# Kernel optimization log

Measured on AMD Instinct MI355X. Metric: run time of the kernel, lower is better.

## Reference

```python
import jax, jax.numpy as jnp
import numpy as np

DEPTH = 4096
BATCH = 16384


def fwht(x):
    """Normalized fast Walsh-Hadamard transform along the last axis.
    x: [B, n], n a power of two. Returns H @ x rows, scaled by 1/sqrt(n).
    """
    B, n = x.shape
    h = 1
    while h < n:
        # combine elements i and i+h within blocks of size 2h (butterfly)
        x = x.reshape(B, n // (2 * h), 2, h)
        a = x[..., 0, :]
        b = x[..., 1, :]
        x = jnp.concatenate([a + b, a - b], axis=-1).reshape(B, n)
        h *= 2
    return x * (1.0 / jnp.sqrt(jnp.asarray(n, x.dtype)))


def setup_inputs() -> dict:
    key = jax.random.key(0)
    kx, kp = jax.random.split(key)
    x = jax.random.normal(kx, (BATCH, DEPTH), dtype=jnp.float32)
    # learned diagonal vectors S, G, B initialized to ones as in the module
    diag_s = jnp.ones((DEPTH,), dtype=jnp.float32)
    diag_g = jnp.ones((DEPTH,), dtype=jnp.float32)
    diag_b = jnp.ones((DEPTH,), dtype=jnp.float32)
    # random permutation: torch.mm(y, P) with P a row-permuted identity is a
    # column gather y[:, idx] for idx = argsort(pi); idx itself is a uniform
    # random permutation, so we draw it directly.
    perm_idx = jax.random.permutation(kp, jnp.arange(DEPTH, dtype=jnp.int32))
    return {"x": x, "diag_s": diag_s, "diag_g": diag_g, "diag_b": diag_b,
            "perm_idx": perm_idx}


def reference(x, diag_s, diag_g, diag_b, perm_idx):
    # forward: S * H * G * P * H * B  (dropout in eval mode -> identity)
    y = x * diag_b                 # mul_b: diagonal scale
    y = fwht(y)                    # first Walsh-Hadamard transform
    y = jnp.take(y, perm_idx, axis=1)  # mul_p: column permutation
    y = y * diag_g                 # mul_g
    y = fwht(y)                    # second Walsh-Hadamard transform
    y = y * diag_s                 # mul_s
    return y
```

## Files before the change

### kernel.cpp

```cpp
#include <hip/hip_runtime.h>

#define FF_N 4096
#define S64  0.015625f

typedef float v2f __attribute__((ext_vector_type(2)));

__device__ __forceinline__ v2f pk_add(v2f a, v2f b) {
    v2f d; asm("v_pk_add_f32 %0, %1, %2" : "=v"(d) : "v"(a), "v"(b)); return d;
}
__device__ __forceinline__ v2f pk_sub(v2f a, v2f b) {
    v2f d; asm("v_pk_add_f32 %0, %1, %2 neg_lo:[0,1] neg_hi:[0,1]"
               : "=v"(d) : "v"(a), "v"(b)); return d;
}

__device__ __forceinline__ void h16p(v2f v[16]) {
#pragma unroll
    for (int b = 1; b < 16; b <<= 1) {
#pragma unroll
        for (int r = 0; r < 16; ++r) {
            if ((r & b) == 0) {
                const v2f u = v[r], w = v[r | b];
                v[r]     = pk_add(u, w);
                v[r | b] = pk_sub(u, w);
            }
        }
    }
}

__global__ void ff_setup(const float* __restrict__ diag_s,
                         const float* __restrict__ diag_g,
                         const int*   __restrict__ perm,
                         int*   __restrict__ gaddr2,
                         float* __restrict__ gg,
                         float* __restrict__ ss) {
    const int k   = blockIdx.x * 256 + threadIdx.x;
    const int pe  = perm[k];
    const int d2p = pe >> 8, d1p = (pe >> 4) & 15, d0p = pe & 15;
    gaddr2[k] = 512 * (d2p >> 1) + 32 * d1p + 2 * (d0p ^ ((d2p >> 1) & 7)) + (d2p & 1);
    gg[k] = diag_g[k] * S64;
    ss[k] = diag_s[k] * S64;
}

__global__ __launch_bounds__(256) void fastfood_pk_kernel(
    const float* __restrict__ x,
    const float* __restrict__ diag_b,
    const int*   __restrict__ gaddr2,
    const float* __restrict__ gg,
    const float* __restrict__ ss,
    float* __restrict__ out)
{
    __shared__ __align__(16) v2f lds2[FF_N];
    const int t = threadIdx.x;
    const int T = t >> 4, c = t & 15;
    const int h = c >> 3;
    const size_t rowA = (size_t)blockIdx.x * 2;
    const float* __restrict__ xA   = x   + rowA * FF_N;
    const float* __restrict__ xB   = xA  + FF_N;
    float* __restrict__       outA = out + rowA * FF_N;
    float* __restrict__       outB = outA + FF_N;

    v2f v2[16];

    {
        const float4* __restrict__ xa4 = (const float4*)(xA + 16 * t);
        const float4* __restrict__ xb4 = (const float4*)(xB + 16 * t);
        const float4* __restrict__ b4  = (const float4*)(diag_b + 16 * t);
#pragma unroll
        for (int q = 0; q < 4; ++q) {
            const float4 bv = b4[q];
            const float4 av = xa4[q];
            const float4 wv = xb4[q];
            v2[4 * q + 0][0] = av.x * bv.x;  v2[4 * q + 0][1] = wv.x * bv.x;
            v2[4 * q + 1][0] = av.y * bv.y;  v2[4 * q + 1][1] = wv.y * bv.y;
            v2[4 * q + 2][0] = av.z * bv.z;  v2[4 * q + 2][1] = wv.z * bv.z;
            v2[4 * q + 3][0] = av.w * bv.w;  v2[4 * q + 3][1] = wv.w * bv.w;
        }
        h16p(v2);
#pragma unroll
        for (int m = 0; m < 8; ++m) {
            const int p = 256 * c + 16 * T + 2 * (m ^ (c & 7));
            *(float4*)&lds2[p] = make_float4(v2[2 * m][0], v2[2 * m][1],
                                             v2[2 * m + 1][0], v2[2 * m + 1][1]);
        }
    }
    __syncthreads();

#pragma unroll
    for (int j = 0; j < 16; ++j)
        v2[j] = lds2[256 * j + 16 * T + 2 * ((c >> 1) ^ (j & 7)) + (c & 1)];
    h16p(v2);
    __syncthreads();
#pragma unroll
    for (int m = 0; m < 8; ++m) {
        const int p = 256 * T + 32 * m + 2 * c;
        const v2f lo = h ? v2[2 * m + 1] : v2[2 * m];
        const v2f hi = h ? v2[2 * m]     : v2[2 * m + 1];
        *(float4*)&lds2[p] = make_float4(lo[0], lo[1], hi[0], hi[1]);
    }
    __syncthreads();

#pragma unroll
    for (int j = 0; j < 16; ++j)
        v2[j] = lds2[256 * j + 32 * (T >> 1) + 2 * c + ((T & 1) ^ h)];
    h16p(v2);
    __syncthreads();
#pragma unroll
    for (int mu = 0; mu < 8; ++mu) {
        const int p = 512 * mu + 32 * T + 2 * (c ^ (mu & 7));
        *(float4*)&lds2[p] = make_float4(v2[2 * mu][0], v2[2 * mu][1],
                                         v2[2 * mu + 1][0], v2[2 * mu + 1][1]);
    }
    __syncthreads();

    {
        const int4*   __restrict__ ga4 = (const int4*)(gaddr2 + 16 * t);
        const float4* __restrict__ gg4 = (const float4*)(gg + 16 * t);
#pragma unroll
        for (int q = 0; q < 4; ++q) {
            const int4   pa = ga4[q];
            const float4 gv = gg4[q];
            const v2f a0 = lds2[pa.x], a1 = lds2[pa.y];
            const v2f a2 = lds2[pa.z], a3 = lds2[pa.w];
            v2[4 * q + 0][0] = a0[0] * gv.x;  v2[4 * q + 0][1] = a0[1] * gv.x;
            v2[4 * q + 1][0] = a1[0] * gv.y;  v2[4 * q + 1][1] = a1[1] * gv.y;
            v2[4 * q + 2][0] = a2[0] * gv.z;  v2[4 * q + 2][1] = a2[1] * gv.z;
            v2[4 * q + 3][0] = a3[0] * gv.w;  v2[4 * q + 3][1] = a3[1] * gv.w;
        }
        h16p(v2);
    }
    __syncthreads();
#pragma unroll
    for (int m = 0; m < 8; ++m) {
        const int p = 256 * c + 16 * T + 2 * (m ^ (c & 7));
        *(float4*)&lds2[p] = make_float4(v2[2 * m][0], v2[2 * m][1],
                                         v2[2 * m + 1][0], v2[2 * m + 1][1]);
    }
    __syncthreads();

#pragma unroll
    for (int j = 0; j < 16; ++j)
        v2[j] = lds2[256 * j + 16 * T + 2 * ((c >> 1) ^ (j & 7)) + (c & 1)];
    h16p(v2);
    __syncthreads();
#pragma unroll
    for (int m = 0; m < 8; ++m) {
        const int p = 256 * T + 32 * m + 2 * c;
        const v2f lo = h ? v2[2 * m + 1] : v2[2 * m];
        const v2f hi = h ? v2[2 * m]     : v2[2 * m + 1];
        *(float4*)&lds2[p] = make_float4(lo[0], lo[1], hi[0], hi[1]);
    }
    __syncthreads();

#pragma unroll
    for (int j = 0; j < 16; ++j)
        v2[j] = lds2[256 * j + 32 * (T >> 1) + 2 * c + ((T & 1) ^ h)];
    h16p(v2);
#pragma unroll
    for (int j = 0; j < 16; ++j) {
        const int e = 256 * j + t;
        const float s = ss[e];
        __builtin_nontemporal_store(v2[j][0] * s, &outA[e]);
        __builtin_nontemporal_store(v2[j][1] * s, &outB[e]);
    }
}

extern "C" void kernel_launch(void* const* d_in, const int* in_sizes, int n_in,
                              void* d_out, int out_size, void* d_ws, size_t ws_size,
                              hipStream_t stream) {
    const float* x      = (const float*)d_in[0];
    const float* diag_s = (const float*)d_in[1];
    const float* diag_g = (const float*)d_in[2];
    const float* diag_b = (const float*)d_in[3];
    const int*   perm   = (const int*)d_in[4];
    float* out = (float*)d_out;

    int*   gaddr2 = (int*)d_ws;
    float* gg     = (float*)d_ws + FF_N;
    float* ss     = (float*)d_ws + 2 * FF_N;

    ff_setup<<<FF_N / 256, 256, 0, stream>>>(diag_s, diag_g, perm, gaddr2, gg, ss);

    const int batch = in_sizes[0] / FF_N;
    fastfood_pk_kernel<<<batch / 2, 256, 0, stream>>>(x, diag_b, gaddr2, gg, ss, out);
}
```

Measured before the change: 94.26 us.

## Process four rows per block using two packed LDS buffers

Each block now handles four rows instead of two, keeping two packed register arrays and two 32 KB LDS buffers. The aim is to amortize barriers, the diag_b/gaddr/gg/ss loads and the per-block overhead over twice the work, and to give each wave more independent memory and ALU work between syncs. The cost is doubled LDS (64 KB per block) and register pressure, which lowers occupancy and halves the grid size.

```diff
diff --git a/kernel.cpp b/kernel.cpp
--- a/kernel.cpp
+++ b/kernel.cpp
@@ -24,6 +24,47 @@
                 v[r | b] = pk_sub(u, w);
             }
         }
+    }
+}
+
+__device__ __forceinline__ void a_read(v2f v[16], const v2f* __restrict__ L,
+                                       int T, int c) {
+#pragma unroll
+    for (int j = 0; j < 16; ++j)
+        v[j] = L[256 * j + 16 * T + 2 * ((c >> 1) ^ (j & 7)) + (c & 1)];
+}
+__device__ __forceinline__ void a_write(const v2f v[16], v2f* __restrict__ L,
+                                        int T, int c) {
+#pragma unroll
+    for (int m = 0; m < 8; ++m) {
+        const int p = 256 * c + 16 * T + 2 * (m ^ (c & 7));
+        *(float4*)&L[p] = make_float4(v[2 * m][0], v[2 * m][1],
+                                      v[2 * m + 1][0], v[2 * m + 1][1]);
+    }
+}
+__device__ __forceinline__ void p_read(v2f v[16], const v2f* __restrict__ L,
+                                       int T, int c, int h) {
+#pragma unroll
+    for (int j = 0; j < 16; ++j)
+        v[j] = L[256 * j + 32 * (T >> 1) + 2 * c + ((T & 1) ^ h)];
+}
+__device__ __forceinline__ void p_write(const v2f v[16], v2f* __restrict__ L,
+                                        int T, int c, int h) {
+#pragma unroll
+    for (int m = 0; m < 8; ++m) {
+        const int p = 256 * T + 32 * m + 2 * c;
+        const v2f lo = h ? v[2 * m + 1] : v[2 * m];
+        const v2f hi = h ? v[2 * m]     : v[2 * m + 1];
+        *(float4*)&L[p] = make_float4(lo[0], lo[1], hi[0], hi[1]);
+    }
+}
+__device__ __forceinline__ void w_write(const v2f v[16], v2f* __restrict__ L,
+                                        int T, int c) {
+#pragma unroll
+    for (int mu = 0; mu < 8; ++mu) {
+        const int p = 512 * mu + 32 * T + 2 * (c ^ (mu & 7));
+        *(float4*)&L[p] = make_float4(v[2 * mu][0], v[2 * mu][1],
+                                      v[2 * mu + 1][0], v[2 * mu + 1][1]);
     }
 }
 
@@ -41,7 +82,7 @@
     ss[k] = diag_s[k] * S64;
 }
 
-__global__ __launch_bounds__(256) void fastfood_pk_kernel(
+__global__ __launch_bounds__(256) void fastfood_2p_kernel(
     const float* __restrict__ x,
     const float* __restrict__ diag_b,
     const int*   __restrict__ gaddr2,
@@ -49,67 +90,62 @@
     const float* __restrict__ ss,
     float* __restrict__ out)
 {
-    __shared__ __align__(16) v2f lds2[FF_N];
+    __shared__ __align__(16) v2f LP[FF_N];
+    __shared__ __align__(16) v2f LQ[FF_N];
     const int t = threadIdx.x;
     const int T = t >> 4, c = t & 15;
     const int h = c >> 3;
-    const size_t rowA = (size_t)blockIdx.x * 2;
-    const float* __restrict__ xA   = x   + rowA * FF_N;
-    const float* __restrict__ xB   = xA  + FF_N;
-    float* __restrict__       outA = out + rowA * FF_N;
-    float* __restrict__       outB = outA + FF_N;
-
-    v2f v2[16];
+    const size_t row0 = (size_t)blockIdx.x * 4;
+    const float* __restrict__ xA = x + row0 * FF_N;
+    const float* __restrict__ xB = xA + FF_N;
+    const float* __restrict__ xC = xB + FF_N;
+    const float* __restrict__ xD = xC + FF_N;
+    float* __restrict__ oA = out + row0 * FF_N;
+    float* __restrict__ oB = oA + FF_N;
+    float* __restrict__ oC = oB + FF_N;
+    float* __restrict__ oD = oC + FF_N;
+
+    v2f vP[16], vQ[16];
 
     {
-        const float4* __restrict__ xa4 = (const float4*)(xA + 16 * t);
-        const float4* __restrict__ xb4 = (const float4*)(xB + 16 * t);
-        const float4* __restrict__ b4  = (const float4*)(diag_b + 16 * t);
+        const float4* __restrict__ a4 = (const float4*)(xA + 16 * t);
+        const float4* __restrict__ b4 = (const float4*)(xB + 16 * t);
+        const float4* __restrict__ c4 = (const float4*)(xC + 16 * t);
+        const float4* __restrict__ d4 = (const float4*)(xD + 16 * t);
+        const float4* __restrict__ g4 = (const float4*)(diag_b + 16 * t);
 #pragma unroll
         for (int q = 0; q < 4; ++q) {
-            const float4 bv = b4[q];
-            const float4 av = xa4[q];
-            const float4 wv = xb4[q];
-            v2[4 * q + 0][0] = av.x * bv.x;  v2[4 * q + 0][1] = wv.x * bv.x;
-            v2[4 * q + 1][0] = av.y * bv.y;  v2[4 * q + 1][1] = wv.y * bv.y;
-            v2[4 * q + 2][0] = av.z * bv.z;  v2[4 * q + 2][1] = wv.z * bv.z;
-            v2[4 * q + 3][0] = av.w * bv.w;  v2[4 * q + 3][1] = wv.w * bv.w;
+            const float4 gv = g4[q];
+            const float4 av = a4[q], bv = b4[q], cv = c4[q], dv = d4[q];
+            vP[4 * q + 0][0] = av.x * gv.x;  vP[4 * q + 0][1] = bv.x * gv.x;
+            vP[4 * q + 1][0] = av.y * gv.y;  vP[4 * q + 1][1] = bv.y * gv.y;
+            vP[4 * q + 2][0] = av.z * gv.z;  vP[4 * q + 2][1] = bv.z * gv.z;
+            vP[4 * q + 3][0] = av.w * gv.w;  vP[4 * q + 3][1] = bv.w * gv.w;
+            vQ[4 * q + 0][0] = cv.x * gv.x;  vQ[4 * q + 0][1] = dv.x * gv.x;
+            vQ[4 * q + 1][0] = cv.y * gv.y;  vQ[4 * q + 1][1] = dv.y * gv.y;
+            vQ[4 * q + 2][0] = cv.z * gv.z;  vQ[4 * q + 2][1] = dv.z * gv.z;
+            vQ[4 * q + 3][0] = cv.w * gv.w;  vQ[4 * q + 3][1] = dv.w * gv.w;
         }
-        h16p(v2);
-#pragma unroll
-        for (int m = 0; m < 8; ++m) {
-            const int p = 256 * c + 16 * T + 2 * (m ^ (c & 7));
-            *(float4*)&lds2[p] = make_float4(v2[2 * m][0], v2[2 * m][1],
-                                             v2[2 * m + 1][0], v2[2 * m + 1][1]);
-        }
-    }
-    __syncthreads();
-
-#pragma unroll
-    for (int j = 0; j < 16; ++j)
-        v2[j] = lds2[256 * j + 16 * T + 2 * ((c >> 1) ^ (j & 7)) + (c & 1)];
-    h16p(v2);
-    __syncthreads();
-#pragma unroll
-    for (int m = 0; m < 8; ++m) {
-        const int p = 256 * T + 32 * m + 2 * c;
-        const v2f lo = h ? v2[2 * m + 1] : v2[2 * m];
-        const v2f hi = h ? v2[2 * m]     : v2[2 * m + 1];
-        *(float4*)&lds2[p] = make_float4(lo[0], lo[1], hi[0], hi[1]);
-    }
-    __syncthreads();
-
-#pragma unroll
-    for (int j = 0; j < 16; ++j)
-        v2[j] = lds2[256 * j + 32 * (T >> 1) + 2 * c + ((T & 1) ^ h)];
-    h16p(v2);
-    __syncthreads();
-#pragma unroll
-    for (int mu = 0; mu < 8; ++mu) {
-        const int p = 512 * mu + 32 * T + 2 * (c ^ (mu & 7));
-        *(float4*)&lds2[p] = make_float4(v2[2 * mu][0], v2[2 * mu][1],
-                                         v2[2 * mu + 1][0], v2[2 * mu + 1][1]);
-    }
+        h16p(vP); h16p(vQ);
+        a_write(vP, LP, T, c);
+        a_write(vQ, LQ, T, c);
+    }
+    __syncthreads();
+
+    a_read(vP, LP, T, c);
+    a_read(vQ, LQ, T, c);
+    h16p(vP); h16p(vQ);
+    __syncthreads();
+    p_write(vP, LP, T, c, h);
+    p_write(vQ, LQ, T, c, h);
+    __syncthreads();
+
+    p_read(vP, LP, T, c, h);
+    p_read(vQ, LQ, T, c, h);
+    h16p(vP); h16p(vQ);
+    __syncthreads();
+    w_write(vP, LP, T, c);
+    w_write(vQ, LQ, T, c);
     __syncthreads();
 
     {
@@ -119,48 +155,43 @@
         for (int q = 0; q < 4; ++q) {
             const int4   pa = ga4[q];
             const float4 gv = gg4[q];
-            const v2f a0 = lds2[pa.x], a1 = lds2[pa.y];
-            const v2f a2 = lds2[pa.z], a3 = lds2[pa.w];
-            v2[4 * q + 0][0] = a0[0] * gv.x;  v2[4 * q + 0][1] = a0[1] * gv.x;
-            v2[4 * q + 1][0] = a1[0] * gv.y;  v2[4 * q + 1][1] = a1[1] * gv.y;
-            v2[4 * q + 2][0] = a2[0] * gv.z;  v2[4 * q + 2][1] = a2[1] * gv.z;
-            v2[4 * q + 3][0] = a3[0] * gv.w;  v2[4 * q + 3][1] = a3[1] * gv.w;
+            const v2f p0 = LP[pa.x], p1 = LP[pa.y], p2 = LP[pa.z], p3 = LP[pa.w];
+            const v2f q0 = LQ[pa.x], q1 = LQ[pa.y], q2 = LQ[pa.z], q3 = LQ[pa.w];
+            vP[4 * q + 0][0] = p0[0] * gv.x;  vP[4 * q + 0][1] = p0[1] * gv.x;
+            vP[4 * q + 1][0] = p1[0] * gv.y;  vP[4 * q + 1][1] = p1[1] * gv.y;
+            vP[4 * q + 2][0] = p2[0] * gv.z;  vP[4 * q + 2][1] = p2[1] * gv.z;
+            vP[4 * q + 3][0] = p3[0] * gv.w;  vP[4 * q + 3][1] = p3[1] * gv.w;
+            vQ[4 * q + 0][0] = q0[0] * gv.x;  vQ[4 * q + 0][1] = q0[1] * gv.x;
+            vQ[4 * q + 1][0] = q1[0] * gv.y;  vQ[4 * q + 1][1] = q1[1] * gv.y;
+            vQ[4 * q + 2][0] = q2[0] * gv.z;  vQ[4 * q + 2][1] = q2[1] * gv.z;
+            vQ[4 * q + 3][0] = q3[0] * gv.w;  vQ[4 * q + 3][1] = q3[1] * gv.w;
         }
-        h16p(v2);
-    }
-    __syncthreads();
-#pragma unroll
-    for (int m = 0; m < 8; ++m) {
-        const int p = 256 * c + 16 * T + 2 * (m ^ (c & 7));
-        *(float4*)&lds2[p] = make_float4(v2[2 * m][0], v2[2 * m][1],
-                                         v2[2 * m + 1][0], v2[2 * m + 1][1]);
-    }
-    __syncthreads();
-
-#pragma unroll
-    for (int j = 0; j < 16; ++j)
-        v2[j] = lds2[256 * j + 16 * T + 2 * ((c >> 1) ^ (j & 7)) + (c & 1)];
-    h16p(v2);
-    __syncthreads();
-#pragma unroll
-    for (int m = 0; m < 8; ++m) {
-        const int p = 256 * T + 32 * m + 2 * c;
-        const v2f lo = h ? v2[2 * m + 1] : v2[2 * m];
-        const v2f hi = h ? v2[2 * m]     : v2[2 * m + 1];
-        *(float4*)&lds2[p] = make_float4(lo[0], lo[1], hi[0], hi[1]);
-    }
-    __syncthreads();
-
-#pragma unroll
-    for (int j = 0; j < 16; ++j)
-        v2[j] = lds2[256 * j + 32 * (T >> 1) + 2 * c + ((T & 1) ^ h)];
-    h16p(v2);
+        h16p(vP); h16p(vQ);
+    }
+    __syncthreads();
+    a_write(vP, LP, T, c);
+    a_write(vQ, LQ, T, c);
+    __syncthreads();
+
+    a_read(vP, LP, T, c);
+    a_read(vQ, LQ, T, c);
+    h16p(vP); h16p(vQ);
+    __syncthreads();
+    p_write(vP, LP, T, c, h);
+    p_write(vQ, LQ, T, c, h);
+    __syncthreads();
+
+    p_read(vP, LP, T, c, h);
+    p_read(vQ, LQ, T, c, h);
+    h16p(vP); h16p(vQ);
 #pragma unroll
     for (int j = 0; j < 16; ++j) {
         const int e = 256 * j + t;
         const float s = ss[e];
-        __builtin_nontemporal_store(v2[j][0] * s, &outA[e]);
-        __builtin_nontemporal_store(v2[j][1] * s, &outB[e]);
+        __builtin_nontemporal_store(vP[j][0] * s, &oA[e]);
+        __builtin_nontemporal_store(vP[j][1] * s, &oB[e]);
+        __builtin_nontemporal_store(vQ[j][0] * s, &oC[e]);
+        __builtin_nontemporal_store(vQ[j][1] * s, &oD[e]);
     }
 }
 
@@ -181,5 +212,5 @@
     ff_setup<<<FF_N / 256, 256, 0, stream>>>(diag_s, diag_g, perm, gaddr2, gg, ss);
 
     const int batch = in_sizes[0] / FF_N;
-    fastfood_pk_kernel<<<batch / 2, 256, 0, stream>>>(x, diag_b, gaddr2, gg, ss, out);
-}
+    fastfood_2p_kernel<<<batch / 4, 256, 0, stream>>>(x, diag_b, gaddr2, gg, ss, out);
+}
```

Result: slower. 114.8 us (+21.8%).

## Store inter-stage FWHT data in LDS as packed fp16 pairs

Applied to the files above, without the earlier changes.

Intermediate butterfly results exchanged through shared memory are converted to packed half precision, halving LDS footprint and traffic. The LDS index layout and the permutation address table are redesigned for the 32-bit packed words, with a unified write pattern. Launch bounds now request higher occupancy. This trades accuracy (fp16 rounding at six exchange points) for lower LDS pressure, on a kernel that is largely bound by global memory bandwidth.

```diff
diff --git a/kernel.cpp b/kernel.cpp
--- a/kernel.cpp
+++ b/kernel.cpp
@@ -3,7 +3,8 @@
 #define FF_N 4096
 #define S64  0.015625f
 
-typedef float v2f __attribute__((ext_vector_type(2)));
+typedef float  v2f __attribute__((ext_vector_type(2)));
+typedef __fp16 pkhalf2 __attribute__((ext_vector_type(2)));
 
 __device__ __forceinline__ v2f pk_add(v2f a, v2f b) {
     v2f d; asm("v_pk_add_f32 %0, %1, %2" : "=v"(d) : "v"(a), "v"(b)); return d;
@@ -12,7 +13,6 @@
     v2f d; asm("v_pk_add_f32 %0, %1, %2 neg_lo:[0,1] neg_hi:[0,1]"
                : "=v"(d) : "v"(a), "v"(b)); return d;
 }
-
 __device__ __forceinline__ void h16p(v2f v[16]) {
 #pragma unroll
     for (int b = 1; b < 16; b <<= 1) {
@@ -27,39 +27,69 @@
     }
 }
 
+__device__ __forceinline__ unsigned pkpack(v2f a) {
+    union { pkhalf2 h; unsigned u; } cv;
+    cv.h = __builtin_amdgcn_cvt_pkrtz(a[0], a[1]);
+    return cv.u;
+}
+__device__ __forceinline__ v2f pkunpack(unsigned u) {
+    union { unsigned u; pkhalf2 h; } cv; cv.u = u;
+    return (v2f){(float)cv.h[0], (float)cv.h[1]};
+}
+
+
 __global__ void ff_setup(const float* __restrict__ diag_s,
                          const float* __restrict__ diag_g,
                          const int*   __restrict__ perm,
-                         int*   __restrict__ gaddr2,
+                         int*   __restrict__ gaddr,
                          float* __restrict__ gg,
                          float* __restrict__ ss) {
     const int k   = blockIdx.x * 256 + threadIdx.x;
     const int pe  = perm[k];
     const int d2p = pe >> 8, d1p = (pe >> 4) & 15, d0p = pe & 15;
-    gaddr2[k] = 512 * (d2p >> 1) + 32 * d1p + 2 * (d0p ^ ((d2p >> 1) & 7)) + (d2p & 1);
+    gaddr[k] = (d1p << 8) | ((d0p >> 3) << 7) | ((d2p >> 2) << 5)
+             | (((d0p & 7) ^ (d2p >> 2)) << 2) | (d2p & 3);
     gg[k] = diag_g[k] * S64;
     ss[k] = diag_s[k] * S64;
 }
 
-__global__ __launch_bounds__(256) void fastfood_pk_kernel(
+__global__ __launch_bounds__(256, 6) void fastfood_h16_kernel(
     const float* __restrict__ x,
     const float* __restrict__ diag_b,
-    const int*   __restrict__ gaddr2,
+    const int*   __restrict__ gaddr,
     const float* __restrict__ gg,
     const float* __restrict__ ss,
     float* __restrict__ out)
 {
-    __shared__ __align__(16) v2f lds2[FF_N];
+    __shared__ __align__(16) unsigned L[FF_N];
     const int t = threadIdx.x;
     const int T = t >> 4, c = t & 15;
-    const int h = c >> 3;
     const size_t rowA = (size_t)blockIdx.x * 2;
     const float* __restrict__ xA   = x   + rowA * FF_N;
     const float* __restrict__ xB   = xA  + FF_N;
     float* __restrict__       outA = out + rowA * FF_N;
     float* __restrict__       outB = outA + FF_N;
 
-    v2f v2[16];
+    int WB[4];
+#pragma unroll
+    for (int q = 0; q < 4; ++q)
+        WB[q] = (T << 8) | ((c >> 3) << 7) | (q << 5) | ((((c & 7) ^ q)) << 2);
+    const int AR0 = (T << 8) | ((c >> 2) << 5) | (c & 3);
+    const int PR0 = ((c >> 3) << 7) | ((T >> 2) << 5)
+                  | ((((c & 7) ^ (T >> 2))) << 2) | (T & 3);
+
+    v2f v[16];
+
+#define JWRITE()                                                               \
+    {                                                                          \
+        _Pragma("unroll")                                                      \
+        for (int q = 0; q < 4; ++q) {                                          \
+            uint4 w;                                                           \
+            w.x = pkpack(v[4 * q + 0]); w.y = pkpack(v[4 * q + 1]);            \
+            w.z = pkpack(v[4 * q + 2]); w.w = pkpack(v[4 * q + 3]);            \
+            *(uint4*)&L[WB[q]] = w;                                            \
+        }                                                                      \
+    }
 
     {
         const float4* __restrict__ xa4 = (const float4*)(xA + 16 * t);
@@ -70,98 +100,72 @@
             const float4 bv = b4[q];
             const float4 av = xa4[q];
             const float4 wv = xb4[q];
-            v2[4 * q + 0][0] = av.x * bv.x;  v2[4 * q + 0][1] = wv.x * bv.x;
-            v2[4 * q + 1][0] = av.y * bv.y;  v2[4 * q + 1][1] = wv.y * bv.y;
-            v2[4 * q + 2][0] = av.z * bv.z;  v2[4 * q + 2][1] = wv.z * bv.z;
-            v2[4 * q + 3][0] = av.w * bv.w;  v2[4 * q + 3][1] = wv.w * bv.w;
+            v[4 * q + 0] = (v2f){av.x * bv.x, wv.x * bv.x};
+            v[4 * q + 1] = (v2f){av.y * bv.y, wv.y * bv.y};
+            v[4 * q + 2] = (v2f){av.z * bv.z, wv.z * bv.z};
+            v[4 * q + 3] = (v2f){av.w * bv.w, wv.w * bv.w};
         }
-        h16p(v2);
-#pragma unroll
-        for (int m = 0; m < 8; ++m) {
-            const int p = 256 * c + 16 * T + 2 * (m ^ (c & 7));
-            *(float4*)&lds2[p] = make_float4(v2[2 * m][0], v2[2 * m][1],
-                                             v2[2 * m + 1][0], v2[2 * m + 1][1]);
-        }
+        h16p(v);
+        JWRITE();
     }
     __syncthreads();
 
 #pragma unroll
     for (int j = 0; j < 16; ++j)
-        v2[j] = lds2[256 * j + 16 * T + 2 * ((c >> 1) ^ (j & 7)) + (c & 1)];
-    h16p(v2);
+        v[j] = pkunpack(L[AR0 | ((j >> 3) << 7) | ((((j & 7) ^ (c >> 2))) << 2)]);
+    h16p(v);
     __syncthreads();
-#pragma unroll
-    for (int m = 0; m < 8; ++m) {
-        const int p = 256 * T + 32 * m + 2 * c;
-        const v2f lo = h ? v2[2 * m + 1] : v2[2 * m];
-        const v2f hi = h ? v2[2 * m]     : v2[2 * m + 1];
-        *(float4*)&lds2[p] = make_float4(lo[0], lo[1], hi[0], hi[1]);
-    }
+    JWRITE();
     __syncthreads();
 
 #pragma unroll
     for (int j = 0; j < 16; ++j)
-        v2[j] = lds2[256 * j + 32 * (T >> 1) + 2 * c + ((T & 1) ^ h)];
-    h16p(v2);
+        v[j] = pkunpack(L[PR0 | (j << 8)]);
+    h16p(v);
     __syncthreads();
-#pragma unroll
-    for (int mu = 0; mu < 8; ++mu) {
-        const int p = 512 * mu + 32 * T + 2 * (c ^ (mu & 7));
-        *(float4*)&lds2[p] = make_float4(v2[2 * mu][0], v2[2 * mu][1],
-                                         v2[2 * mu + 1][0], v2[2 * mu + 1][1]);
-    }
+    JWRITE();
     __syncthreads();
 
     {
-        const int4*   __restrict__ ga4 = (const int4*)(gaddr2 + 16 * t);
+        const int4*   __restrict__ ga4 = (const int4*)(gaddr + 16 * t);
         const float4* __restrict__ gg4 = (const float4*)(gg + 16 * t);
 #pragma unroll
         for (int q = 0; q < 4; ++q) {
             const int4   pa = ga4[q];
             const float4 gv = gg4[q];
-            const v2f a0 = lds2[pa.x], a1 = lds2[pa.y];
-            const v2f a2 = lds2[pa.z], a3 = lds2[pa.w];
-            v2[4 * q + 0][0] = a0[0] * gv.x;  v2[4 * q + 0][1] = a0[1] * gv.x;
-            v2[4 * q + 1][0] = a1[0] * gv.y;  v2[4 * q + 1][1] = a1[1] * gv.y;
-            v2[4 * q + 2][0] = a2[0] * gv.z;  v2[4 * q + 2][1] = a2[1] * gv.z;
-            v2[4 * q + 3][0] = a3[0] * gv.w;  v2[4 * q + 3][1] = a3[1] * gv.w;
+            const v2f a0 = pkunpack(L[pa.x]), a1 = pkunpack(L[pa.y]);
+            const v2f a2 = pkunpack(L[pa.z]), a3 = pkunpack(L[pa.w]);
+            v[4 * q + 0] = (v2f){a0[0] * gv.x, a0[1] * gv.x};
+            v[4 * q + 1] = (v2f){a1[0] * gv.y, a1[1] * gv.y};
+            v[4 * q + 2] = (v2f){a2[0] * gv.z, a2[1] * gv.z};
+            v[4 * q + 3] = (v2f){a3[0] * gv.w, a3[1] * gv.w};
         }
-        h16p(v2);
+        h16p(v);
     }
     __syncthreads();
-#pragma unroll
-    for (int m = 0; m < 8; ++m) {
-        const int p = 256 * c + 16 * T + 2 * (m ^ (c & 7));
-        *(float4*)&lds2[p] = make_float4(v2[2 * m][0], v2[2 * m][1],
-                                         v2[2 * m + 1][0], v2[2 * m + 1][1]);
-    }
+    JWRITE();
     __syncthreads();
 
 #pragma unroll
     for (int j = 0; j < 16; ++j)
-        v2[j] = lds2[256 * j + 16 * T + 2 * ((c >> 1) ^ (j & 7)) + (c & 1)];
-    h16p(v2);
+        v[j] = pkunpack(L[AR0 | ((j >> 3) << 7) | ((((j & 7) ^ (c >> 2))) << 2)]);
+    h16p(v);
     __syncthreads();
-#pragma unroll
-    for (int m = 0; m < 8; ++m) {
-        const int p = 256 * T + 32 * m + 2 * c;
-        const v2f lo = h ? v2[2 * m + 1] : v2[2 * m];
-        const v2f hi = h ? v2[2 * m]     : v2[2 * m + 1];
-        *(float4*)&lds2[p] = make_float4(lo[0], lo[1], hi[0], hi[1]);
-    }
+    JWRITE();
     __syncthreads();
 
 #pragma unroll
     for (int j = 0; j < 16; ++j)
-        v2[j] = lds2[256 * j + 32 * (T >> 1) + 2 * c + ((T & 1) ^ h)];
-    h16p(v2);
+        v[j] = pkunpack(L[PR0 | (j << 8)]);
+    h16p(v);
 #pragma unroll
     for (int j = 0; j < 16; ++j) {
         const int e = 256 * j + t;
         const float s = ss[e];
-        __builtin_nontemporal_store(v2[j][0] * s, &outA[e]);
-        __builtin_nontemporal_store(v2[j][1] * s, &outB[e]);
+        __builtin_nontemporal_store(v[j][0] * s, &outA[e]);
+        __builtin_nontemporal_store(v[j][1] * s, &outB[e]);
     }
+#undef JWRITE
 }
 
 extern "C" void kernel_launch(void* const* d_in, const int* in_sizes, int n_in,
@@ -174,12 +178,12 @@
     const int*   perm   = (const int*)d_in[4];
     float* out = (float*)d_out;
 
-    int*   gaddr2 = (int*)d_ws;
-    float* gg     = (float*)d_ws + FF_N;
-    float* ss     = (float*)d_ws + 2 * FF_N;
+    int*   gaddr = (int*)d_ws;
+    float* gg    = (float*)d_ws + FF_N;
+    float* ss    = (float*)d_ws + 2 * FF_N;
 
-    ff_setup<<<FF_N / 256, 256, 0, stream>>>(diag_s, diag_g, perm, gaddr2, gg, ss);
+    ff_setup<<<FF_N / 256, 256, 0, stream>>>(diag_s, diag_g, perm, gaddr, gg, ss);
 
     const int batch = in_sizes[0] / FF_N;
-    fastfood_pk_kernel<<<batch / 2, 256, 0, stream>>>(x, diag_b, gaddr2, gg, ss, out);
+    fastfood_h16_kernel<<<batch / 2, 256, 0, stream>>>(x, diag_b, gaddr, gg, ss, out);
 }
```

New measurement: 93.10 us. No clear change (-1.2%).
